# Kernel tuning notes

Measured on AMD Instinct MI355X. Metric: run time of the kernel, lower is better.

The kernel has to match this reference:

```python
import jax, jax.numpy as jnp
import numpy as np

N_NODES = 50000


def _gcn_layer(x, src, dst, W, b, n_nodes):
    # PyG GCNConv: h = x @ W, add self-loops, sym-normalized scatter-add, + bias
    h = x @ W  # [N, Dout]
    loop = jnp.arange(n_nodes, dtype=src.dtype)
    src2 = jnp.concatenate([src, loop])
    dst2 = jnp.concatenate([dst, loop])
    ones = jnp.ones(src2.shape[0], dtype=x.dtype)
    deg = jax.ops.segment_sum(ones, dst2, num_segments=n_nodes)  # in-degree w/ self-loops
    dinv = jnp.where(deg > 0, jax.lax.rsqrt(deg), 0.0)
    norm = dinv[src2] * dinv[dst2]  # [E+N]
    msg = h[src2] * norm[:, None]   # gather + scale
    out = jax.ops.segment_sum(msg, dst2, num_segments=n_nodes)  # scatter-add
    return out + b


def setup_inputs() -> dict:
    key = jax.random.key(0)
    k1, k2, k3, k4 = jax.random.split(key, 4)
    x = jax.random.normal(k1, (N_NODES, 128), dtype=jnp.float32)
    edge_index = jax.random.randint(k2, (2, 500000), 0, N_NODES, dtype=jnp.int64)
    W1 = jax.random.normal(k3, (128, 128), dtype=jnp.float32) * (1.0 / np.sqrt(128))
    b1 = jnp.zeros((128,), dtype=jnp.float32)
    W2 = jax.random.normal(k4, (128, 64), dtype=jnp.float32) * (1.0 / np.sqrt(128))
    b2 = jnp.zeros((64,), dtype=jnp.float32)
    return {"x": x, "edge_index": edge_index, "W1": W1, "b1": b1, "W2": W2, "b2": b2}


def reference(x, edge_index, W1, b1, W2, b2):
    src, dst = edge_index[0], edge_index[1]
    n = x.shape[0]
    h = _gcn_layer(x, src, dst, W1, b1, n)
    h = jax.nn.relu(h)
    out = _gcn_layer(h, src, dst, W2, b2, n)
    return out
```

## Files before the change

kernel.cpp:

```cpp
#include <hip/hip_runtime.h>
#include <hip/hip_bf16.h>
#include <cstddef>


typedef __attribute__((ext_vector_type(8))) short short8;
typedef __attribute__((ext_vector_type(4))) float f32x4;
typedef unsigned long long u64;

__device__ inline unsigned short f2bf(float f) {
    __hip_bfloat16 b = __float2bfloat16(f);
    return *reinterpret_cast<unsigned short*>(&b);
}
__device__ inline float bf2f_lo(unsigned int u) {
    unsigned int v = u << 16;
    return *reinterpret_cast<float*>(&v);
}
__device__ inline float bf2f_hi(unsigned int u) {
    unsigned int v = u & 0xffff0000u;
    return *reinterpret_cast<float*>(&v);
}
__device__ inline u64 ld_acq64(u64* p) {
    return __hip_atomic_load(p, __ATOMIC_ACQUIRE, __HIP_MEMORY_SCOPE_AGENT);
}
__device__ inline void st_rel64(u64* p, u64 v) {
    __hip_atomic_store(p, v, __ATOMIC_RELEASE, __HIP_MEMORY_SCOPE_AGENT);
}

__global__ __launch_bounds__(256) void init_kernel(const float* __restrict__ W1,
                                                   const float* __restrict__ W2,
                                                   unsigned short* __restrict__ W1f,
                                                   unsigned short* __restrict__ W2f,
                                                   int* __restrict__ deg,
                                                   u64* __restrict__ lb, int N) {
    int idx = blockIdx.x * 256 + threadIdx.x;
    if (idx < N) deg[idx] = 0;
    if (idx < 64) lb[idx] = 0;
    if (idx < 3072) {
        const float* W;
        unsigned short* Wf;
        int n, oct, Nc;
        if (idx < 2048) { W = W1; Wf = W1f; Nc = 128; n = idx >> 4; oct = idx & 15; }
        else { W = W2; Wf = W2f; Nc = 64; int i2 = idx - 2048; n = i2 >> 4; oct = i2 & 15; }
        int k0 = oct * 8;
        int ks = k0 >> 5, quad = (k0 >> 3) & 3, ntg = n >> 4;
        short8 v;
        #pragma unroll
        for (int j = 0; j < 8; j++) v[j] = (short)f2bf(W[(k0 + j) * Nc + n]);
        int off = (((ntg * 4 + ks) * 64) + (n & 15) + 16 * quad) * 8;
        *(short8*)(Wf + off) = v;
    }
}

__global__ __launch_bounds__(256) void count_kernel(const int* __restrict__ dst, int E,
                                                    int* __restrict__ deg) {
    int i = blockIdx.x * blockDim.x + threadIdx.x;
    if (i < E) atomicAdd(&deg[dst[i]], 1);
}

__global__ __launch_bounds__(256) void scan_lb_kernel(const int* __restrict__ deg, int N,
                                                      u64* __restrict__ lb,
                                                      int* __restrict__ offs,
                                                      int* __restrict__ cur,
                                                      float* __restrict__ dinv) {
    __shared__ int ws[4];
    __shared__ int s_prefix;
    int tid = threadIdx.x;
    int sb = blockIdx.x;
    int SB = gridDim.x;
    int lane = tid & 63;
    int wv = tid >> 6;

    int i = sb * 1024 + tid * 4;
    int v0 = (i + 0 < N) ? deg[i + 0] : 0;
    int v1 = (i + 1 < N) ? deg[i + 1] : 0;
    int v2 = (i + 2 < N) ? deg[i + 2] : 0;
    int v3 = (i + 3 < N) ? deg[i + 3] : 0;
    int tsum = v0 + v1 + v2 + v3;
    int xs = tsum;
    #pragma unroll
    for (int off = 1; off < 64; off <<= 1) {
        int y = __shfl_up(xs, off, 64);
        if (lane >= off) xs += y;
    }
    if (lane == 63) ws[wv] = xs;
    __syncthreads();
    int wprefix = 0;
    #pragma unroll
    for (int w2 = 0; w2 < 4; w2++) wprefix += (w2 < wv) ? ws[w2] : 0;
    int chunk_total = ws[0] + ws[1] + ws[2] + ws[3];

    if (tid == 0) {
        st_rel64(&lb[sb], ((u64)(unsigned)chunk_total << 2) | 1ull);
        int prefix = 0;
        for (int pred = sb - 1; pred >= 0; --pred) {
            u64 v;
            do {
                v = ld_acq64(&lb[pred]);
                if ((v & 3) == 0) __builtin_amdgcn_s_sleep(1);
            } while ((v & 3) == 0);
            prefix += (int)(unsigned)(v >> 2);
            if ((v & 3) == 2) break;
        }
        st_rel64(&lb[sb], ((u64)(unsigned)(prefix + chunk_total) << 2) | 2ull);
        s_prefix = prefix;
    }
    __syncthreads();

    int carry = s_prefix;
    int e0 = carry + wprefix + xs - tsum;
    int e1 = e0 + v0, e2 = e1 + v1, e3 = e2 + v2;
    if (i + 0 < N) { offs[i + 0] = e0; cur[i + 0] = e0; dinv[i + 0] = rsqrtf((float)(v0 + 1)); }
    if (i + 1 < N) { offs[i + 1] = e1; cur[i + 1] = e1; dinv[i + 1] = rsqrtf((float)(v1 + 1)); }
    if (i + 2 < N) { offs[i + 2] = e2; cur[i + 2] = e2; dinv[i + 2] = rsqrtf((float)(v2 + 1)); }
    if (i + 3 < N) { offs[i + 3] = e3; cur[i + 3] = e3; dinv[i + 3] = rsqrtf((float)(v3 + 1)); }
    if (sb == SB - 1 && tid == 0) offs[N] = carry + chunk_total;
}

__global__ __launch_bounds__(256) void fillgemm_kernel(
    const float* __restrict__ x, const unsigned short* __restrict__ W1f,
    unsigned short* __restrict__ h1, int N,
    const int* __restrict__ src, const int* __restrict__ dst, int E,
    int* __restrict__ cur, const float* __restrict__ dinv,
    unsigned int* __restrict__ csr) {

    const int GB = (N + 63) / 64;
    int b = blockIdx.x;
    int tid = threadIdx.x;

    __shared__ unsigned short As[64 * 128];

    if (b >= GB) {
        int i = (b - GB) * 256 + tid;
        if (i < E) {
            int s = src[i];
            int d = dst[i];
            int p = atomicAdd(&cur[d], 1);
            float w = dinv[s] * dinv[d];
            csr[i >= 0 ? p : 0] = (unsigned int)s | ((unsigned int)f2bf(w) << 16);
        }
        return;
    }

    constexpr int K = 128, BN = 128;
    int lane = tid & 63;
    int w = tid >> 6;
    int row0 = b * 64;

    short8 bfr[2][4];
    #pragma unroll
    for (int nl = 0; nl < 2; nl++)
        #pragma unroll
        for (int ks = 0; ks < 4; ks++)
            bfr[nl][ks] = *(const short8*)(W1f + ((((w * 2 + nl) * 4 + ks) * 64) + lane) * 8);

    #pragma unroll
    for (int it = 0; it < 8; it++) {
        int idx = it * 256 + tid;
        int row = idx >> 5, kq = idx & 31;
        int k0 = kq * 4;
        int ks = k0 >> 5, quad = (k0 >> 3) & 3, j0 = k0 & 7, mt = row >> 4;
        ushort4 o = make_ushort4(0, 0, 0, 0);
        int gr = row0 + row;
        if (gr < N) {
            float4 a = *(const float4*)(x + (size_t)gr * K + k0);
            o.x = f2bf(a.x); o.y = f2bf(a.y); o.z = f2bf(a.z); o.w = f2bf(a.w);
        }
        int off = (((mt * 4 + ks) * 64) + (row & 15) + 16 * quad) * 8 + j0;
        *(ushort4*)(As + off) = o;
    }
    __syncthreads();

    f32x4 acc[4][2];
    #pragma unroll
    for (int mt = 0; mt < 4; mt++)
        #pragma unroll
        for (int nl = 0; nl < 2; nl++) acc[mt][nl] = (f32x4){0.f, 0.f, 0.f, 0.f};

    #pragma unroll
    for (int ks = 0; ks < 4; ks++) {
        short8 af[4];
        #pragma unroll
        for (int mt = 0; mt < 4; mt++)
            af[mt] = *(const short8*)(As + (((mt * 4 + ks) * 64) + lane) * 8);
        #pragma unroll
        for (int mt = 0; mt < 4; mt++)
            #pragma unroll
            for (int nl = 0; nl < 2; nl++)
                acc[mt][nl] = __builtin_amdgcn_mfma_f32_16x16x32_bf16(
                    af[mt], bfr[nl][ks], acc[mt][nl], 0, 0, 0);
    }

    int col16 = lane & 15;
    int rowq = lane >> 4;
    #pragma unroll
    for (int mt = 0; mt < 4; mt++) {
        #pragma unroll
        for (int nl = 0; nl < 2; nl++) {
            int gc = (w * 2 + nl) * 16 + col16;
            #pragma unroll
            for (int r = 0; r < 4; r++) {
                int gr = row0 + mt * 16 + rowq * 4 + r;
                if (gr < N) h1[(size_t)gr * BN + gc] = f2bf(acc[mt][nl][r]);
            }
        }
    }
}

__global__ __launch_bounds__(256) void aggmm_kernel(const unsigned short* __restrict__ h1,
                                                    const int* __restrict__ offs,
                                                    const unsigned int* __restrict__ csr,
                                                    const float* __restrict__ dinv,
                                                    const float* __restrict__ b1,
                                                    const unsigned short* __restrict__ W2f,
                                                    unsigned short* __restrict__ h2,
                                                    int n) {
    __shared__ unsigned short As[4 * 64 * 8];

    int tid = threadIdx.x;
    int t = tid & 63;
    int w = tid >> 6;
    int p = t >> 5;
    int t5 = t & 31;
    int nodebase = blockIdx.x * 16;

    short8 bw[4];
    #pragma unroll
    for (int ks = 0; ks < 4; ks++)
        bw[ks] = *(const short8*)(W2f + (((w * 4 + ks) * 64) + t) * 8);

    float4 bias = *(const float4*)(b1 + t5 * 4);

    #pragma unroll
    for (int i = 0; i < 4; i++) {
        int row16 = w * 4 + i;
        int node = nodebase + row16;
        float a0 = 0.f, a1 = 0.f, a2 = 0.f, a3 = 0.f;
        if (node < n) {
            float di = dinv[node];
            float sw = di * di;
            if (p == 0) {
                uint2 su = *(const uint2*)(h1 + (size_t)node * 128 + t5 * 4);
                a0 = bf2f_lo(su.x) * sw; a1 = bf2f_hi(su.x) * sw;
                a2 = bf2f_lo(su.y) * sw; a3 = bf2f_hi(su.y) * sw;
            }
            int e0 = offs[node];
            int e1 = offs[node + 1];
            int iters = (e1 - e0 + 7) >> 3;
            for (int it = 0; it < iters; it++) {
                int eb = e0 + it * 8;
                #pragma unroll
                for (int j = 0; j < 4; j++) {
                    int ee = eb + j * 2 + p;
                    int ec = min(ee, e1 - 1);
                    unsigned int pk = csr[ec];
                    float wgt = (ee < e1) ? bf2f_hi(pk) : 0.f;
                    int s = pk & 0xffff;
                    uint2 hu = *(const uint2*)(h1 + (size_t)s * 128 + t5 * 4);
                    a0 += bf2f_lo(hu.x) * wgt; a1 += bf2f_hi(hu.x) * wgt;
                    a2 += bf2f_lo(hu.y) * wgt; a3 += bf2f_hi(hu.y) * wgt;
                }
            }
        }
        a0 += __shfl_xor(a0, 32, 64);
        a1 += __shfl_xor(a1, 32, 64);
        a2 += __shfl_xor(a2, 32, 64);
        a3 += __shfl_xor(a3, 32, 64);
        if (p == 0) {
            if (node < n) {
                a0 = fmaxf(a0 + bias.x, 0.f);
                a1 = fmaxf(a1 + bias.y, 0.f);
                a2 = fmaxf(a2 + bias.z, 0.f);
                a3 = fmaxf(a3 + bias.w, 0.f);
            }
            int k0 = t5 * 4;
            int ks = k0 >> 5, quad = (k0 >> 3) & 3, j0 = k0 & 7;
            ushort4 pk4 = make_ushort4(f2bf(a0), f2bf(a1), f2bf(a2), f2bf(a3));
            *(ushort4*)(As + ((ks * 64) + row16 + 16 * quad) * 8 + j0) = pk4;
        }
    }
    __syncthreads();

    f32x4 acc = (f32x4){0.f, 0.f, 0.f, 0.f};
    #pragma unroll
    for (int ks = 0; ks < 4; ks++) {
        short8 af = *(const short8*)(As + ((ks * 64) + t) * 8);
        acc = __builtin_amdgcn_mfma_f32_16x16x32_bf16(af, bw[ks], acc, 0, 0, 0);
    }

    int col = w * 16 + (t & 15);
    int rowq = t >> 4;
    #pragma unroll
    for (int r = 0; r < 4; r++) {
        int gr = nodebase + rowq * 4 + r;
        if (gr < n) h2[(size_t)gr * 64 + col] = f2bf(acc[r]);
    }
}

__global__ __launch_bounds__(256) void aggout_kernel(const unsigned short* __restrict__ h2,
                                                     const int* __restrict__ offs,
                                                     const unsigned int* __restrict__ csr,
                                                     const float* __restrict__ dinv,
                                                     const float* __restrict__ b2,
                                                     float* __restrict__ out, int n) {
    int tid = threadIdx.x;
    int t = tid & 63;
    int w = tid >> 6;
    int node = blockIdx.x * 4 + w;
    if (node >= n) return;
    int p = t >> 4;
    int t4 = t & 15;

    float a0 = 0.f, a1 = 0.f, a2 = 0.f, a3 = 0.f;
    float di = dinv[node];
    float sw = di * di;
    if (p == 0) {
        uint2 su = *(const uint2*)(h2 + (size_t)node * 64 + t4 * 4);
        a0 = bf2f_lo(su.x) * sw; a1 = bf2f_hi(su.x) * sw;
        a2 = bf2f_lo(su.y) * sw; a3 = bf2f_hi(su.y) * sw;
    }

    int e0 = offs[node];
    int e1 = offs[node + 1];
    int iters = (e1 - e0 + 7) >> 3;
    for (int it = 0; it < iters; it++) {
        int eb = e0 + it * 8;
        #pragma unroll
        for (int j = 0; j < 2; j++) {
            int ee = eb + j * 4 + p;
            int ec = min(ee, e1 - 1);
            unsigned int pk = csr[ec];
            float wgt = (ee < e1) ? bf2f_hi(pk) : 0.f;
            int s = pk & 0xffff;
            uint2 hu = *(const uint2*)(h2 + (size_t)s * 64 + t4 * 4);
            a0 += bf2f_lo(hu.x) * wgt; a1 += bf2f_hi(hu.x) * wgt;
            a2 += bf2f_lo(hu.y) * wgt; a3 += bf2f_hi(hu.y) * wgt;
        }
    }
    a0 += __shfl_xor(a0, 16, 64); a1 += __shfl_xor(a1, 16, 64);
    a2 += __shfl_xor(a2, 16, 64); a3 += __shfl_xor(a3, 16, 64);
    a0 += __shfl_xor(a0, 32, 64); a1 += __shfl_xor(a1, 32, 64);
    a2 += __shfl_xor(a2, 32, 64); a3 += __shfl_xor(a3, 32, 64);
    if (p == 0) {
        float4 bb = *(const float4*)(b2 + t4 * 4);
        *(float4*)(out + (size_t)node * 64 + t4 * 4) =
            make_float4(a0 + bb.x, a1 + bb.y, a2 + bb.z, a3 + bb.w);
    }
}

extern "C" void kernel_launch(void* const* d_in, const int* in_sizes, int n_in,
                              void* d_out, int out_size, void* d_ws, size_t ws_size,
                              hipStream_t stream) {
    const float* x  = (const float*)d_in[0];
    const int*   ei = (const int*)d_in[1];
    const float* W1 = (const float*)d_in[2];
    const float* b1 = (const float*)d_in[3];
    const float* W2 = (const float*)d_in[4];
    const float* b2 = (const float*)d_in[5];

    const int N = in_sizes[0] / 128;
    const int E = in_sizes[1] / 2;
    const int* src = ei;
    const int* dst = ei + E;

    char* p = (char*)d_ws;
    auto alloc = [&](size_t bytes) {
        char* r = p;
        p += (bytes + 255) & ~(size_t)255;
        return r;
    };
    int*   degi  = (int*)  alloc((size_t)N * 4);
    float* dinv  = (float*)alloc((size_t)N * 4);
    int*   offs  = (int*)  alloc((size_t)(N + 1) * 4);
    int*   cur   = (int*)  alloc((size_t)N * 4);
    u64*   lb    = (u64*)  alloc((size_t)64 * 8);
    unsigned int*   csr  = (unsigned int*)alloc((size_t)E * 4);
    unsigned short* W1f  = (unsigned short*)alloc((size_t)128 * 128 * 2);
    unsigned short* W2f  = (unsigned short*)alloc((size_t)64 * 128 * 2);
    unsigned short* h1   = (unsigned short*)alloc((size_t)N * 128 * 2);
    unsigned short* h2   = (unsigned short*)alloc((size_t)N * 64 * 2);
    float* out = (float*)d_out;

    const int GB = (N + 63) / 64;
    const int FB = (E + 255) / 256;
    const int SB = (N + 1023) / 1024;

    init_kernel<<<(N + 255) / 256, 256, 0, stream>>>(W1, W2, W1f, W2f, degi, lb, N);
    count_kernel<<<FB, 256, 0, stream>>>(dst, E, degi);
    scan_lb_kernel<<<SB, 256, 0, stream>>>(degi, N, lb, offs, cur, dinv);
    fillgemm_kernel<<<GB + FB, 256, 0, stream>>>(x, W1f, h1, N, src, dst, E,
                                                 cur, dinv, csr);
    aggmm_kernel<<<(N + 15) / 16, 256, 0, stream>>>(h1, offs, csr, dinv, b1, W2f, h2, N);
    aggout_kernel<<<(N + 3) / 4, 256, 0, stream>>>(h2, offs, csr, dinv, b2, out, N);
}
```

Baseline: 190.9 us.

## Factor symmetric normalization into GEMM epilogues and shrink CSR to 16-bit indices

```diff
diff --git a/kernel.cpp b/kernel.cpp
--- a/kernel.cpp
+++ b/kernel.cpp
@@ -53,8 +53,16 @@
 
 __global__ __launch_bounds__(256) void count_kernel(const int* __restrict__ dst, int E,
                                                     int* __restrict__ deg) {
-    int i = blockIdx.x * blockDim.x + threadIdx.x;
-    if (i < E) atomicAdd(&deg[dst[i]], 1);
+    int i = (blockIdx.x * blockDim.x + threadIdx.x) * 4;
+    if (i + 3 < E) {
+        int4 d = *(const int4*)(dst + i);
+        atomicAdd(&deg[d.x], 1);
+        atomicAdd(&deg[d.y], 1);
+        atomicAdd(&deg[d.z], 1);
+        atomicAdd(&deg[d.w], 1);
+    } else {
+        for (; i < E; i++) atomicAdd(&deg[dst[i]], 1);
+    }
 }
 
 __global__ __launch_bounds__(256) void scan_lb_kernel(const int* __restrict__ deg, int N,
@@ -121,22 +129,22 @@
     unsigned short* __restrict__ h1, int N,
     const int* __restrict__ src, const int* __restrict__ dst, int E,
     int* __restrict__ cur, const float* __restrict__ dinv,
-    unsigned int* __restrict__ csr) {
-
-    const int GB = (N + 63) / 64;
+    unsigned short* __restrict__ csr) {
+
+    const int FB = (E + 255) / 256;
     int b = blockIdx.x;
     int tid = threadIdx.x;
 
     __shared__ unsigned short As[64 * 128];
-
-    if (b >= GB) {
-        int i = (b - GB) * 256 + tid;
+    __shared__ float sdinv[64];
+
+    if (b < FB) {
+        int i = b * 256 + tid;
         if (i < E) {
             int s = src[i];
             int d = dst[i];
             int p = atomicAdd(&cur[d], 1);
-            float w = dinv[s] * dinv[d];
-            csr[i >= 0 ? p : 0] = (unsigned int)s | ((unsigned int)f2bf(w) << 16);
+            csr[p] = (unsigned short)s;
         }
         return;
     }
@@ -144,7 +152,12 @@
     constexpr int K = 128, BN = 128;
     int lane = tid & 63;
     int w = tid >> 6;
-    int row0 = b * 64;
+    int row0 = (b - FB) * 64;
+
+    if (tid < 64) {
+        int gr = row0 + tid;
+        sdinv[tid] = (gr < N) ? dinv[gr] : 0.f;
+    }
 
     short8 bfr[2][4];
     #pragma unroll
@@ -199,8 +212,9 @@
             int gc = (w * 2 + nl) * 16 + col16;
             #pragma unroll
             for (int r = 0; r < 4; r++) {
-                int gr = row0 + mt * 16 + rowq * 4 + r;
-                if (gr < N) h1[(size_t)gr * BN + gc] = f2bf(acc[mt][nl][r]);
+                int lr = mt * 16 + rowq * 4 + r;
+                int gr = row0 + lr;
+                if (gr < N) C_STORE: h1[(size_t)gr * BN + gc] = f2bf(acc[mt][nl][r] * sdinv[lr]);
             }
         }
     }
@@ -208,7 +222,7 @@
 
 __global__ __launch_bounds__(256) void aggmm_kernel(const unsigned short* __restrict__ h1,
                                                     const int* __restrict__ offs,
-                                                    const unsigned int* __restrict__ csr,
+                                                    const unsigned short* __restrict__ csr,
                                                     const float* __restrict__ dinv,
                                                     const float* __restrict__ b1,
                                                     const unsigned short* __restrict__ W2f,
@@ -235,13 +249,13 @@
         int row16 = w * 4 + i;
         int node = nodebase + row16;
         float a0 = 0.f, a1 = 0.f, a2 = 0.f, a3 = 0.f;
+        float di = 0.f;
         if (node < n) {
-            float di = dinv[node];
-            float sw = di * di;
+            di = dinv[node];
             if (p == 0) {
                 uint2 su = *(const uint2*)(h1 + (size_t)node * 128 + t5 * 4);
-                a0 = bf2f_lo(su.x) * sw; a1 = bf2f_hi(su.x) * sw;
-                a2 = bf2f_lo(su.y) * sw; a3 = bf2f_hi(su.y) * sw;
+                a0 = bf2f_lo(su.x); a1 = bf2f_hi(su.x);
+                a2 = bf2f_lo(su.y); a3 = bf2f_hi(su.y);
             }
             int e0 = offs[node];
             int e1 = offs[node + 1];
@@ -252,9 +266,8 @@
                 for (int j = 0; j < 4; j++) {
                     int ee = eb + j * 2 + p;
                     int ec = min(ee, e1 - 1);
-                    unsigned int pk = csr[ec];
-                    float wgt = (ee < e1) ? bf2f_hi(pk) : 0.f;
-                    int s = pk & 0xffff;
+                    int s = csr[ec];
+                    float wgt = (ee < e1) ? 1.f : 0.f;
                     uint2 hu = *(const uint2*)(h1 + (size_t)s * 128 + t5 * 4);
                     a0 += bf2f_lo(hu.x) * wgt; a1 += bf2f_hi(hu.x) * wgt;
                     a2 += bf2f_lo(hu.y) * wgt; a3 += bf2f_hi(hu.y) * wgt;
@@ -267,10 +280,10 @@
         a3 += __shfl_xor(a3, 32, 64);
         if (p == 0) {
             if (node < n) {
-                a0 = fmaxf(a0 + bias.x, 0.f);
-                a1 = fmaxf(a1 + bias.y, 0.f);
-                a2 = fmaxf(a2 + bias.z, 0.f);
-                a3 = fmaxf(a3 + bias.w, 0.f);
+                a0 = fmaxf(a0 * di + bias.x, 0.f);
+                a1 = fmaxf(a1 * di + bias.y, 0.f);
+                a2 = fmaxf(a2 * di + bias.z, 0.f);
+                a3 = fmaxf(a3 * di + bias.w, 0.f);
             }
             int k0 = t5 * 4;
             int ks = k0 >> 5, quad = (k0 >> 3) & 3, j0 = k0 & 7;
@@ -292,13 +305,13 @@
     #pragma unroll
     for (int r = 0; r < 4; r++) {
         int gr = nodebase + rowq * 4 + r;
-        if (gr < n) h2[(size_t)gr * 64 + col] = f2bf(acc[r]);
+        if (gr < n) h2[(size_t)gr * 64 + col] = f2bf(acc[r] * dinv[gr]);
     }
 }
 
 __global__ __launch_bounds__(256) void aggout_kernel(const unsigned short* __restrict__ h2,
                                                      const int* __restrict__ offs,
-                                                     const unsigned int* __restrict__ csr,
+                                                     const unsigned short* __restrict__ csr,
                                                      const float* __restrict__ dinv,
                                                      const float* __restrict__ b2,
                                                      float* __restrict__ out, int n) {
@@ -312,11 +325,10 @@
 
     float a0 = 0.f, a1 = 0.f, a2 = 0.f, a3 = 0.f;
     float di = dinv[node];
-    float sw = di * di;
     if (p == 0) {
         uint2 su = *(const uint2*)(h2 + (size_t)node * 64 + t4 * 4);
-        a0 = bf2f_lo(su.x) * sw; a1 = bf2f_hi(su.x) * sw;
-        a2 = bf2f_lo(su.y) * sw; a3 = bf2f_hi(su.y) * sw;
+        a0 = bf2f_lo(su.x); a1 = bf2f_hi(su.x);
+        a2 = bf2f_lo(su.y); a3 = bf2f_hi(su.y);
     }
 
     int e0 = offs[node];
@@ -328,9 +340,8 @@
         for (int j = 0; j < 2; j++) {
             int ee = eb + j * 4 + p;
             int ec = min(ee, e1 - 1);
-            unsigned int pk = csr[ec];
-            float wgt = (ee < e1) ? bf2f_hi(pk) : 0.f;
-            int s = pk & 0xffff;
+            int s = csr[ec];
+            float wgt = (ee < e1) ? 1.f : 0.f;
             uint2 hu = *(const uint2*)(h2 + (size_t)s * 64 + t4 * 4);
             a0 += bf2f_lo(hu.x) * wgt; a1 += bf2f_hi(hu.x) * wgt;
             a2 += bf2f_lo(hu.y) * wgt; a3 += bf2f_hi(hu.y) * wgt;
@@ -343,7 +354,7 @@
     if (p == 0) {
         float4 bb = *(const float4*)(b2 + t4 * 4);
         *(float4*)(out + (size_t)node * 64 + t4 * 4) =
-            make_float4(a0 + bb.x, a1 + bb.y, a2 + bb.z, a3 + bb.w);
+            make_float4(a0 * di + bb.x, a1 * di + bb.y, a2 * di + bb.z, a3 * di + bb.w);
     }
 }
 
@@ -373,7 +384,7 @@
     int*   offs  = (int*)  alloc((size_t)(N + 1) * 4);
     int*   cur   = (int*)  alloc((size_t)N * 4);
     u64*   lb    = (u64*)  alloc((size_t)64 * 8);
-    unsigned int*   csr  = (unsigned int*)alloc((size_t)E * 4);
+    unsigned short* csr  = (unsigned short*)alloc((size_t)E * 2);
     unsigned short* W1f  = (unsigned short*)alloc((size_t)128 * 128 * 2);
     unsigned short* W2f  = (unsigned short*)alloc((size_t)64 * 128 * 2);
     unsigned short* h1   = (unsigned short*)alloc((size_t)N * 128 * 2);
@@ -383,11 +394,12 @@
     const int GB = (N + 63) / 64;
     const int FB = (E + 255) / 256;
     const int SB = (N + 1023) / 1024;
+    const int CB = (E / 4 + 255) / 256;
 
     init_kernel<<<(N + 255) / 256, 256, 0, stream>>>(W1, W2, W1f, W2f, degi, lb, N);
-    count_kernel<<<FB, 256, 0, stream>>>(dst, E, degi);
+    count_kernel<<<CB, 256, 0, stream>>>(dst, E, degi);
     scan_lb_kernel<<<SB, 256, 0, stream>>>(degi, N, lb, offs, cur, dinv);
-    fillgemm_kernel<<<GB + FB, 256, 0, stream>>>(x, W1f, h1, N, src, dst, E,
+    fillgemm_kernel<<<FB + GB, 256, 0, stream>>>(x, W1f, h1, N, src, dst, E,
                                                  cur, dinv, csr);
     aggmm_kernel<<<(N + 15) / 16, 256, 0, stream>>>(h1, offs, csr, dinv, b1, W2f, h2, N);
     aggout_kernel<<<(N + 3) / 4, 256, 0, stream>>>(h2, offs, csr, dinv, b2, out, N);
```

Measured after the change: 195.0 us. +2.2%, slower.
